# Performance work log

Measured on AMD Instinct MI355X. Metric: run time of the kernel, lower is better.

## Reference

```python
import jax, jax.numpy as jnp
import numpy as np

BIG = 1e10  # stand-in for excluding masked rows from the min (safe for vjp)


def setup_inputs() -> dict:
    key = jax.random.key(0)
    k1, k2 = jax.random.split(key)
    # projected points: mostly inside the 640x480 image, some outside so the mask matters
    proj = jax.random.uniform(k1, (16384, 2), dtype=jnp.float32)
    proj = proj * jnp.array([700.0, 520.0], jnp.float32) - jnp.array([30.0, 20.0], jnp.float32)
    # reference centerline points, inside the image
    ref = jax.random.uniform(k2, (8192, 2), dtype=jnp.float32)
    ref = ref * jnp.array([640.0, 480.0], jnp.float32)
    return {"bezier_proj_centerline_img": proj, "ref_catheter_centerline": ref}


def reference(bezier_proj_centerline_img, ref_catheter_centerline):
    # torch .flip(1) on [M,2] swaps (x,y); .flip(0) on [N,2] reverses point order
    ref = ref_catheter_centerline[:, ::-1]            # [M, 2]
    proj = bezier_proj_centerline_img[::-1, :]        # [N, 2]

    # in-image mask (torch version drops rows; we keep static shapes and mask)
    mask = (
        (proj[:, 0] >= 0.0) & (proj[:, 0] <= 640.0)
        & (proj[:, 1] >= 0.0) & (proj[:, 1] <= 480.0)
    )  # [N]

    # pairwise L2 distances [N, M]
    diff = proj[:, None, :] - ref[None, :, :]         # [N, M, 2]
    dist = jnp.sqrt(jnp.sum(diff * diff, axis=-1))    # [N, M]

    # exclude invalid projected points from both reductions
    dist_masked = jnp.where(mask[:, None], dist, BIG)

    min1 = jnp.min(dist_masked, axis=1)               # [N] nearest ref per proj point
    n_valid = jnp.sum(mask.astype(dist.dtype))
    mean1 = jnp.sum(jnp.where(mask, min1, 0.0)) / n_valid

    min2 = jnp.min(dist_masked, axis=0)               # [M] nearest valid proj per ref point
    mean2 = jnp.mean(min2)

    return (mean1 + mean2) * 0.5
```

## Files before the change

kernel.cpp:

```cpp
#include <hip/hip_runtime.h>


constexpr int NP = 16384;
constexpr int NR = 8192;
constexpr int CH = 256;
constexpr int S1 = NR / CH;
constexpr int S2 = NP / CH;
constexpr int BLK1 = NP / 1024;
constexpr int BLK2 = NR / 1024;
constexpr int G1 = BLK1 * S1;
constexpr int G2 = BLK2 * S2;
constexpr float FMAX = 3.4e38f;

__global__ __launch_bounds__(256) void k_prep(const float* __restrict__ proj,
                                              const float* __restrict__ ref,
                                              float4* __restrict__ kproj,
                                              float4* __restrict__ kref) {
    int i = blockIdx.x * 256 + threadIdx.x;
    float2 p = ((const float2*)proj)[i];
    bool valid = (p.x >= 0.f) && (p.x <= 640.f) && (p.y >= 0.f) && (p.y <= 480.f);
    float pc = fmaf(p.x, p.x, p.y * p.y);
    kproj[i] = valid ? make_float4(-2.f * p.x, -2.f * p.y, pc, 0.f)
                     : make_float4(0.f, 0.f, 1e30f, 0.f);
    if (i < NR) {
        float2 r = ((const float2*)ref)[i];
        kref[i] = make_float4(-2.f * r.y, -2.f * r.x, fmaf(r.x, r.x, r.y * r.y), 0.f);
    }
}

__global__ __launch_bounds__(256) void k_pair(const float* __restrict__ proj,
                                              const float* __restrict__ ref,
                                              const float4* __restrict__ kproj,
                                              const float4* __restrict__ kref,
                                              float* __restrict__ part1,
                                              float* __restrict__ part2) {
    __shared__ float4 sh[CH];
    int tid = threadIdx.x;
    int bx = blockIdx.x;
    bool d1 = bx < G1;
    int cb = d1 ? bx : bx - G1;
    int nbm = (d1 ? BLK1 : BLK2) - 1;
    int pb = cb & nbm;
    int ck = cb >> (d1 ? 4 : 3);

    const float4* keys = d1 ? kref : kproj;
    sh[tid] = keys[ck * CH + tid];
    __syncthreads();

    int base = pb * 1024 + tid;
    const float2* qsrc = (const float2*)(d1 ? proj : ref);
    float2 q0 = qsrc[base];
    float2 q1 = qsrc[base + 256];
    float2 q2 = qsrc[base + 512];
    float2 q3 = qsrc[base + 768];
    if (!d1) {
        float t;
        t = q0.x; q0.x = q0.y; q0.y = t;
        t = q1.x; q1.x = q1.y; q1.y = t;
        t = q2.x; q2.x = q2.y; q2.y = t;
        t = q3.x; q3.x = q3.y; q3.y = t;
    }

    float ma0 = FMAX, mb0 = FMAX, ma1 = FMAX, mb1 = FMAX;
    float ma2 = FMAX, mb2 = FMAX, ma3 = FMAX, mb3 = FMAX;
#pragma unroll 4
    for (int j = 0; j < CH; j += 4) {
        float4 k0 = sh[j], k1 = sh[j + 1], k2 = sh[j + 2], k3 = sh[j + 3];
        float t00 = fmaf(k0.y, q0.y, fmaf(k0.x, q0.x, k0.z));
        float t01 = fmaf(k1.y, q0.y, fmaf(k1.x, q0.x, k1.z));
        float t02 = fmaf(k2.y, q0.y, fmaf(k2.x, q0.x, k2.z));
        float t03 = fmaf(k3.y, q0.y, fmaf(k3.x, q0.x, k3.z));
        ma0 = fminf(fminf(ma0, t00), t01);
        mb0 = fminf(fminf(mb0, t02), t03);
        float t10 = fmaf(k0.y, q1.y, fmaf(k0.x, q1.x, k0.z));
        float t11 = fmaf(k1.y, q1.y, fmaf(k1.x, q1.x, k1.z));
        float t12 = fmaf(k2.y, q1.y, fmaf(k2.x, q1.x, k2.z));
        float t13 = fmaf(k3.y, q1.y, fmaf(k3.x, q1.x, k3.z));
        ma1 = fminf(fminf(ma1, t10), t11);
        mb1 = fminf(fminf(mb1, t12), t13);
        float t20 = fmaf(k0.y, q2.y, fmaf(k0.x, q2.x, k0.z));
        float t21 = fmaf(k1.y, q2.y, fmaf(k1.x, q2.x, k1.z));
        float t22 = fmaf(k2.y, q2.y, fmaf(k2.x, q2.x, k2.z));
        float t23 = fmaf(k3.y, q2.y, fmaf(k3.x, q2.x, k3.z));
        ma2 = fminf(fminf(ma2, t20), t21);
        mb2 = fminf(fminf(mb2, t22), t23);
        float t30 = fmaf(k0.y, q3.y, fmaf(k0.x, q3.x, k0.z));
        float t31 = fmaf(k1.y, q3.y, fmaf(k1.x, q3.x, k1.z));
        float t32 = fmaf(k2.y, q3.y, fmaf(k2.x, q3.x, k2.z));
        float t33 = fmaf(k3.y, q3.y, fmaf(k3.x, q3.x, k3.z));
        ma3 = fminf(fminf(ma3, t30), t31);
        mb3 = fminf(fminf(mb3, t32), t33);
    }

    float* part = d1 ? part1 : part2;
    int n = d1 ? NP : NR;
    part[ck * n + base]       = fminf(ma0, mb0);
    part[ck * n + base + 256] = fminf(ma1, mb1);
    part[ck * n + base + 512] = fminf(ma2, mb2);
    part[ck * n + base + 768] = fminf(ma3, mb3);
}

__global__ __launch_bounds__(256) void k_combine(const float* __restrict__ proj,
                                                 const float* __restrict__ ref,
                                                 const float* __restrict__ part1,
                                                 const float* __restrict__ part2,
                                                 float* __restrict__ bsum1,
                                                 float* __restrict__ bcnt1,
                                                 float* __restrict__ bsum2) {
    __shared__ float red[256];
    __shared__ float redc[256];
    int tid = threadIdx.x;
    int b = blockIdx.x;
    if (b < 64) {
        int i = b * 256 + tid;
        float m = FMAX;
        for (int c = 0; c < S1; ++c) m = fminf(m, part1[c * NP + i]);
        float2 p = ((const float2*)proj)[i];
        bool valid = (p.x >= 0.f) && (p.x <= 640.f) && (p.y >= 0.f) && (p.y <= 480.f);
        float d = sqrtf(fmaxf(m + fmaf(p.x, p.x, p.y * p.y), 0.f));
        red[tid]  = valid ? d : 0.f;
        redc[tid] = valid ? 1.f : 0.f;
        __syncthreads();
        for (int w = 128; w > 0; w >>= 1) {
            if (tid < w) { red[tid] += red[tid + w]; redc[tid] += redc[tid + w]; }
            __syncthreads();
        }
        if (tid == 0) { bsum1[b] = red[0]; bcnt1[b] = redc[0]; }
    } else {
        int j = (b - 64) * 256 + tid;
        float m = FMAX;
        for (int c = 0; c < S2; ++c) m = fminf(m, part2[c * NR + j]);
        float2 r = ((const float2*)ref)[j];
        red[tid] = sqrtf(fmaxf(m + fmaf(r.x, r.x, r.y * r.y), 0.f));
        __syncthreads();
        for (int w = 128; w > 0; w >>= 1) {
            if (tid < w) red[tid] += red[tid + w];
            __syncthreads();
        }
        if (tid == 0) bsum2[b - 64] = red[0];
    }
}

__global__ void k_final(const float* __restrict__ bsum1,
                        const float* __restrict__ bcnt1,
                        const float* __restrict__ bsum2,
                        float* __restrict__ out) {
    float s1 = 0.f, c1 = 0.f, s2 = 0.f;
    for (int b = 0; b < 64; ++b) { s1 += bsum1[b]; c1 += bcnt1[b]; }
    for (int b = 0; b < 32; ++b) s2 += bsum2[b];
    out[0] = 0.5f * (s1 / c1 + s2 / (float)NR);
}

extern "C" void kernel_launch(void* const* d_in, const int* in_sizes, int n_in,
                              void* d_out, int out_size, void* d_ws, size_t ws_size,
                              hipStream_t stream) {
    const float* proj = (const float*)d_in[0];
    const float* ref  = (const float*)d_in[1];
    float* out = (float*)d_out;

    float* ws = (float*)d_ws;
    float4* kproj = (float4*)ws;
    float4* kref  = kproj + NP;
    float*  part1 = (float*)(kref + NR);
    float*  part2 = part1 + S1 * NP;
    float*  bsum1 = part2 + S2 * NR;
    float*  bcnt1 = bsum1 + 64;
    float*  bsum2 = bcnt1 + 64;

    k_prep<<<NP / 256, 256, 0, stream>>>(proj, ref, kproj, kref);
    k_pair<<<G1 + G2, 256, 0, stream>>>(proj, ref, kproj, kref, part1, part2);
    k_combine<<<96, 256, 0, stream>>>(proj, ref, part1, part2, bsum1, bcnt1, bsum2);
    k_final<<<1, 1, 0, stream>>>(bsum1, bcnt1, bsum2, out);
}
```

Measured before the change: 45.54 us.

## Fuse key prep into pair kernel and final reduce into combine via last-block atomic

Key precomputation (scaled coordinates, squared norms, mask sentinel) now happens while each pair block loads its shared-memory tile, so the separate prep kernel and its workspace round trip go away. The single-thread final kernel is replaced by a last-block-done pattern in the combine kernel, using an atomic counter that the pair kernel resets. This cuts four launches to two. In exchange, each pair block recomputes its key tile redundantly, and correctness depends on the counter reset in k_pair being ordered before k_combine on the same stream.

```diff
diff --git a/kernel.cpp b/kernel.cpp
--- a/kernel.cpp
+++ b/kernel.cpp
@@ -12,39 +12,31 @@
 constexpr int G2 = BLK2 * S2;
 constexpr float FMAX = 3.4e38f;
 
-__global__ __launch_bounds__(256) void k_prep(const float* __restrict__ proj,
-                                              const float* __restrict__ ref,
-                                              float4* __restrict__ kproj,
-                                              float4* __restrict__ kref) {
-    int i = blockIdx.x * 256 + threadIdx.x;
-    float2 p = ((const float2*)proj)[i];
-    bool valid = (p.x >= 0.f) && (p.x <= 640.f) && (p.y >= 0.f) && (p.y <= 480.f);
-    float pc = fmaf(p.x, p.x, p.y * p.y);
-    kproj[i] = valid ? make_float4(-2.f * p.x, -2.f * p.y, pc, 0.f)
-                     : make_float4(0.f, 0.f, 1e30f, 0.f);
-    if (i < NR) {
-        float2 r = ((const float2*)ref)[i];
-        kref[i] = make_float4(-2.f * r.y, -2.f * r.x, fmaf(r.x, r.x, r.y * r.y), 0.f);
-    }
-}
-
 __global__ __launch_bounds__(256) void k_pair(const float* __restrict__ proj,
                                               const float* __restrict__ ref,
-                                              const float4* __restrict__ kproj,
-                                              const float4* __restrict__ kref,
                                               float* __restrict__ part1,
-                                              float* __restrict__ part2) {
+                                              float* __restrict__ part2,
+                                              unsigned* __restrict__ counter) {
     __shared__ float4 sh[CH];
     int tid = threadIdx.x;
     int bx = blockIdx.x;
+    if (bx == 0 && tid == 0) *counter = 0u;
+
     bool d1 = bx < G1;
     int cb = d1 ? bx : bx - G1;
-    int nbm = (d1 ? BLK1 : BLK2) - 1;
-    int pb = cb & nbm;
+    int pb = cb & ((d1 ? BLK1 : BLK2) - 1);
     int ck = cb >> (d1 ? 4 : 3);
 
-    const float4* keys = d1 ? kref : kproj;
-    sh[tid] = keys[ck * CH + tid];
+    int kidx = ck * CH + tid;
+    if (d1) {
+        float2 r = ((const float2*)ref)[kidx];
+        sh[tid] = make_float4(-2.f * r.y, -2.f * r.x, fmaf(r.x, r.x, r.y * r.y), 0.f);
+    } else {
+        float2 p = ((const float2*)proj)[kidx];
+        bool valid = (p.x >= 0.f) && (p.x <= 640.f) && (p.y >= 0.f) && (p.y <= 480.f);
+        sh[tid] = valid ? make_float4(-2.f * p.x, -2.f * p.y, fmaf(p.x, p.x, p.y * p.y), 0.f)
+                        : make_float4(0.f, 0.f, 1e30f, 0.f);
+    }
     __syncthreads();
 
     int base = pb * 1024 + tid;
@@ -106,9 +98,12 @@
                                                  const float* __restrict__ part2,
                                                  float* __restrict__ bsum1,
                                                  float* __restrict__ bcnt1,
-                                                 float* __restrict__ bsum2) {
+                                                 float* __restrict__ bsum2,
+                                                 unsigned* __restrict__ counter,
+                                                 float* __restrict__ out) {
     __shared__ float red[256];
     __shared__ float redc[256];
+    __shared__ bool amLast;
     int tid = threadIdx.x;
     int b = blockIdx.x;
     if (b < 64) {
@@ -139,16 +134,35 @@
         }
         if (tid == 0) bsum2[b - 64] = red[0];
     }
-}
 
-__global__ void k_final(const float* __restrict__ bsum1,
-                        const float* __restrict__ bcnt1,
-                        const float* __restrict__ bsum2,
-                        float* __restrict__ out) {
-    float s1 = 0.f, c1 = 0.f, s2 = 0.f;
-    for (int b = 0; b < 64; ++b) { s1 += bsum1[b]; c1 += bcnt1[b]; }
-    for (int b = 0; b < 32; ++b) s2 += bsum2[b];
-    out[0] = 0.5f * (s1 / c1 + s2 / (float)NR);
+    __threadfence();
+    if (tid == 0) {
+        unsigned old = atomicAdd(counter, 1u);
+        amLast = (old == 95u);
+    }
+    __syncthreads();
+    if (amLast) {
+        __threadfence();
+        float v1 = (tid < 64) ? bsum1[tid] : 0.f;
+        float vc = (tid < 64) ? bcnt1[tid] : 0.f;
+        float v2 = (tid < 32) ? bsum2[tid] : 0.f;
+        red[tid] = v1;
+        redc[tid] = vc;
+        __syncthreads();
+        for (int w = 128; w > 0; w >>= 1) {
+            if (tid < w) { red[tid] += red[tid + w]; redc[tid] += redc[tid + w]; }
+            __syncthreads();
+        }
+        float s1 = red[0], c1 = redc[0];
+        __syncthreads();
+        red[tid] = v2;
+        __syncthreads();
+        for (int w = 128; w > 0; w >>= 1) {
+            if (tid < w) red[tid] += red[tid + w];
+            __syncthreads();
+        }
+        if (tid == 0) out[0] = 0.5f * (s1 / c1 + red[0] / (float)NR);
+    }
 }
 
 extern "C" void kernel_launch(void* const* d_in, const int* in_sizes, int n_in,
@@ -159,16 +173,14 @@
     float* out = (float*)d_out;
 
     float* ws = (float*)d_ws;
-    float4* kproj = (float4*)ws;
-    float4* kref  = kproj + NP;
-    float*  part1 = (float*)(kref + NR);
-    float*  part2 = part1 + S1 * NP;
-    float*  bsum1 = part2 + S2 * NR;
-    float*  bcnt1 = bsum1 + 64;
-    float*  bsum2 = bcnt1 + 64;
+    float*    part1   = ws;
+    float*    part2   = part1 + S1 * NP;
+    float*    bsum1   = part2 + S2 * NR;
+    float*    bcnt1   = bsum1 + 64;
+    float*    bsum2   = bcnt1 + 64;
+    unsigned* counter = (unsigned*)(bsum2 + 32);
 
-    k_prep<<<NP / 256, 256, 0, stream>>>(proj, ref, kproj, kref);
-    k_pair<<<G1 + G2, 256, 0, stream>>>(proj, ref, kproj, kref, part1, part2);
-    k_combine<<<96, 256, 0, stream>>>(proj, ref, part1, part2, bsum1, bcnt1, bsum2);
-    k_final<<<1, 1, 0, stream>>>(bsum1, bcnt1, bsum2, out);
+    k_pair<<<G1 + G2, 256, 0, stream>>>(proj, ref, part1, part2, counter);
+    k_combine<<<96, 256, 0, stream>>>(proj, ref, part1, part2,
+                                      bsum1, bcnt1, bsum2, counter, out);
 }
```

New measurement: 45.58 us. About the same (+0.1%).
